# Kernel tuning notes

Measured on AMD Instinct MI355X. Metric: run time of the kernel, lower is better.

The kernel has to match this reference:

```python
import jax, jax.numpy as jnp
import numpy as np
from jax import lax

N_QUBITS = 4
N_QLAYERS = 2
C64 = jnp.complex64
PAIRS = [(i, j) for i in range(N_QUBITS) for j in range(i + 1, N_QUBITS)]  # 6 entangling pairs
CNOT = jnp.array([[1, 0, 0, 0], [0, 1, 0, 0], [0, 0, 0, 1], [0, 0, 1, 0]], dtype=C64)


def _rx(t):
    c = jnp.cos(t / 2).astype(C64)
    s = (-1j * jnp.sin(t / 2)).astype(C64)
    return jnp.stack([jnp.stack([c, s]), jnp.stack([s, c])])


def _ry(t):
    c = jnp.cos(t / 2).astype(C64)
    s = jnp.sin(t / 2).astype(C64)
    return jnp.stack([jnp.stack([c, -s]), jnp.stack([s, c])])


def _rz(t):
    e = jnp.exp(-1j * t.astype(C64) / 2)
    z = jnp.zeros_like(e)
    return jnp.stack([jnp.stack([e, z]), jnp.stack([z, jnp.conj(e)])])


def _apply_1q(state, M, w):
    # state: (B,2,2,2,2); M: (2,2) shared or (B,2,2) per-sample
    s = jnp.moveaxis(state, 1 + w, -1)
    if M.ndim == 2:
        s = jnp.einsum('b...j,ij->b...i', s, M)
    else:
        s = jnp.einsum('b...j,bij->b...i', s, M)
    return jnp.moveaxis(s, -1, 1 + w)


def _apply_2q(state, M4, c, t):
    # M4: (4,4) acting on (wire c, wire t)
    s = jnp.moveaxis(state, (1 + c, 1 + t), (-2, -1))
    sh = s.shape
    s = s.reshape(sh[:-2] + (4,))
    s = jnp.einsum('b...j,ij->b...i', s, M4)
    s = s.reshape(sh)
    return jnp.moveaxis(s, (-2, -1), (1 + c, 1 + t))


def _quantum_batched(angles, q_params):
    # angles: (B, 4) classical outputs; encoding is RY(angles*pi)
    B = angles.shape[0]
    state = jnp.zeros((B, 16), C64).at[:, 0].set(1.0).reshape(B, 2, 2, 2, 2)
    theta = angles * jnp.float32(np.pi)
    c = jnp.cos(theta / 2).astype(C64)  # (B,4)
    s = jnp.sin(theta / 2).astype(C64)
    for w in range(N_QUBITS):
        M = jnp.stack([jnp.stack([c[:, w], -s[:, w]], -1),
                       jnp.stack([s[:, w], c[:, w]], -1)], -2)  # (B,2,2)
        state = _apply_1q(state, M, w)
    per_layer = 3 * N_QUBITS + len(PAIRS)  # 18
    for l in range(N_QLAYERS):
        start = l * per_layer
        rot = q_params[start:start + 3 * N_QUBITS].reshape(N_QUBITS, 3)
        ent = q_params[start + 3 * N_QUBITS:start + per_layer]
        for q in range(N_QUBITS):
            M = _rz(rot[q, 2]) @ _ry(rot[q, 1]) @ _rx(rot[q, 0])
            state = _apply_1q(state, M, q)
        for k, (i, j) in enumerate(PAIRS):
            M4 = jnp.kron(jnp.eye(2, dtype=C64), _rz(ent[k])) @ CNOT  # CNOT then RZ on target
            state = _apply_2q(state, M4, i, j)
    probs = jnp.abs(state) ** 2  # (B,2,2,2,2)
    signs = jnp.array([1.0, -1.0], jnp.float32)
    zs = []
    for w in range(N_QUBITS):
        pw = jnp.moveaxis(probs, 1 + w, -1).reshape(B, -1, 2)
        zs.append((pw.sum(1) * signs).sum(-1))
    return jnp.stack(zs, -1)  # (B,4) PauliZ expvals


def _conv(x, w, b):
    y = lax.conv_general_dilated(x, w, (1, 1), ((1, 1), (1, 1)),
                                 dimension_numbers=('NCHW', 'OIHW', 'NCHW'))
    return y + b[None, :, None, None]


def _pool(x):
    return lax.reduce_window(x, -jnp.inf, lax.max, (1, 1, 2, 2), (1, 1, 2, 2), 'VALID')


def setup_inputs() -> dict:
    key = jax.random.key(0)
    ks = jax.random.split(key, 10)
    B = 4096
    return {
        'x': jax.random.normal(ks[0], (B, 1, 28, 28), jnp.float32),
        'conv1_w': jax.random.normal(ks[1], (16, 1, 3, 3), jnp.float32) * 0.1,
        'conv1_b': jax.random.normal(ks[2], (16,), jnp.float32) * 0.1,
        'conv2_w': jax.random.normal(ks[3], (32, 16, 3, 3), jnp.float32) * 0.05,
        'conv2_b': jax.random.normal(ks[4], (32,), jnp.float32) * 0.1,
        'dense_w': jax.random.normal(ks[5], (4, 1568), jnp.float32) * 0.02,
        'dense_b': jax.random.normal(ks[6], (4,), jnp.float32) * 0.1,
        'q_params': jax.random.normal(ks[7], (36,), jnp.float32) * 0.1,
        'post_w': jax.random.normal(ks[8], (10, 4), jnp.float32) * 0.5,
        'post_b': jax.random.normal(ks[9], (10,), jnp.float32) * 0.1,
    }


def reference(x, conv1_w, conv1_b, conv2_w, conv2_b, dense_w, dense_b, q_params, post_w, post_b):
    h = jax.nn.relu(_conv(x, conv1_w, conv1_b))
    h = _pool(h)
    h = jax.nn.relu(_conv(h, conv2_w, conv2_b))
    h = _pool(h)  # (B,32,7,7)
    h = h.reshape(h.shape[0], 32 * 7 * 7)
    # dropout is identity in eval mode
    angles = h @ dense_w.T + dense_b  # (B,4)
    z = _quantum_batched(angles, q_params)  # (B,4)
    return z @ post_w.T + post_b  # (B,10)
```

## Files before the change

### kernel.cpp

```cpp
#include <hip/hip_runtime.h>

#define PI_F 3.14159265358979323846f

typedef _Float16 half2v __attribute__((ext_vector_type(2)));
typedef _Float16 half4v __attribute__((ext_vector_type(4)));
typedef _Float16 half8v __attribute__((ext_vector_type(8)));
typedef float f32x4 __attribute__((ext_vector_type(4)));

struct C2 { float x, y; };
__device__ __forceinline__ C2 cmul(C2 a, C2 b) {
    return C2{a.x * b.x - a.y * b.y, a.x * b.y + a.y * b.x};
}

__device__ __forceinline__ void gate1(float& re, float& im, int l, int w,
                                      C2 m00, C2 m01, C2 m10, C2 m11) {
    int mask = 1 << (3 - w);
    float pre = __shfl_xor(re, mask, 64);
    float pim = __shfl_xor(im, mask, 64);
    bool b = (l & mask) != 0;
    C2 d = b ? m11 : m00;
    C2 o = b ? m10 : m01;
    float nre = d.x * re - d.y * im + o.x * pre - o.y * pim;
    float nim = d.x * im + d.y * re + o.x * pim + o.y * pre;
    re = nre; im = nim;
}

#define WS_C1B 2560
#define WS_GROT 2688
#define WS_GENT 2752

__global__ __launch_bounds__(256) void qnn_prep(
    const float* __restrict__ w1g, const float* __restrict__ w2g,
    const float* __restrict__ qpg, float* __restrict__ ws)
{
    int t = threadIdx.x;
    for (int e = t; e < 640; e += 256) {
        int kstep = e >> 7, rem = e & 127;
        int ntile = rem >> 6, lane = rem & 63;
        int kq = lane >> 4, n = lane & 15;
        int oc = ntile * 16 + n;
        int pi = kstep * 2 + (kq >> 1);
        half8v h;
        #pragma unroll
        for (int jj = 0; jj < 8; ++jj) {
            int ic = (kq & 1) * 8 + jj;
            float v = (pi < 9) ? w2g[oc * 144 + ic * 9 + pi] : 0.f;
            h[jj] = (_Float16)v;
        }
        *(float4*)(ws + e * 4) = __builtin_bit_cast(float4, h);
    }
    if (t < 64) {
        int ky = t >> 4, n = t & 15;
        half4v h;
        #pragma unroll
        for (int j = 0; j < 4; ++j) {
            float v = (ky < 3 && j < 3) ? w1g[n * 9 + ky * 3 + j] : 0.f;
            h[j] = (_Float16)v;
        }
        *(float2*)(ws + WS_C1B + t * 2) = __builtin_bit_cast(float2, h);
    }
    if (t < 8) {
        int layer = t >> 2, q = t & 3;
        int st = layer * 18;
        float a0 = qpg[st + 3 * q], a1 = qpg[st + 3 * q + 1], a2 = qpg[st + 3 * q + 2];
        float cx = cosf(0.5f * a0), sx = sinf(0.5f * a0);
        float cy = cosf(0.5f * a1), sy = sinf(0.5f * a1);
        float cz = cosf(0.5f * a2), sz = sinf(0.5f * a2);
        C2 T00{cy * cx,  sy * sx}, T01{-sy * cx, -cy * sx};
        C2 T10{sy * cx, -cy * sx}, T11{ cy * cx, -sy * sx};
        C2 E0{cz, -sz}, E1{cz, sz};
        C2 m00 = cmul(E0, T00), m01 = cmul(E0, T01);
        C2 m10 = cmul(E1, T10), m11 = cmul(E1, T11);
        float* gm = ws + WS_GROT + t * 8;
        gm[0] = m00.x; gm[1] = m00.y; gm[2] = m01.x; gm[3] = m01.y;
        gm[4] = m10.x; gm[5] = m10.y; gm[6] = m11.x; gm[7] = m11.y;
    }
    if (t >= 32 && t < 44) {
        int k = t - 32;
        float e = qpg[(k / 6) * 18 + 12 + (k % 6)];
        ws[WS_GENT + k * 2]     = cosf(0.5f * e);
        ws[WS_GENT + k * 2 + 1] = sinf(0.5f * e);
    }
}

__global__ __launch_bounds__(256, 5) void qnn_fused(
    const float* __restrict__ xg,
    const float* __restrict__ b1g, const float* __restrict__ b2g,
    const float* __restrict__ dwg, const float* __restrict__ dbg,
    const float* __restrict__ wsc,
    const float* __restrict__ pwg, const float* __restrict__ pbg,
    float* __restrict__ out)
{
    const int b = blockIdx.x;
    const int t = threadIdx.x;
    const int lane = t & 63;
    const int wv = __builtin_amdgcn_readfirstlane(t >> 6);
    const int kq = lane >> 4;
    const int lm = lane & 15;

    __shared__ __align__(16) unsigned xhl[930];
    __shared__ __align__(16) _Float16 p1f[16 * 20 * 16];
    __shared__ __align__(16) float p2[1568];
    __shared__ float ang[4];
    __shared__ float zsh[4];

    half8v bC2[5][2];
    {
        const float4* wsB = (const float4*)wsc;
        #pragma unroll
        for (int ks = 0; ks < 5; ++ks)
            #pragma unroll
            for (int nt = 0; nt < 2; ++nt)
                bC2[ks][nt] = __builtin_bit_cast(half8v, wsB[(ks * 2 + nt) * 64 + lane]);
    }
    half4v bC1 = __builtin_bit_cast(half4v, *(const float2*)(wsc + WS_C1B + lane * 2));
    float bias1 = b1g[lm];
    float b20 = b2g[lm], b21 = b2g[16 + lm];

    const float* xb = xg + (size_t)b * 784;
    for (int j = t; j < 900; j += 256) {
        int y = j / 30, x = j - y * 30;
        float v = 0.f;
        if (y >= 1 && y <= 28 && x >= 1 && x <= 28)
            v = xb[(y - 1) * 28 + (x - 1)];
        _Float16 h = (_Float16)v;
        _Float16 l = (_Float16)(v - (float)h);
        half2v p; p.x = h; p.y = l;
        xhl[j] = __builtin_bit_cast(unsigned, p);
    }
    if (t < 30) xhl[900 + t] = 0u;
    {
        uint4 z4 = {0u, 0u, 0u, 0u};
        uint4* p4 = (uint4*)p1f;
        #pragma unroll
        for (int j = 0; j < 3; ++j) {
            int i = t + j * 256;
            if (i < 640) p4[i] = z4;
        }
    }
    __syncthreads();

    {
        int kyc = (kq < 3) ? kq : 0;
        for (int tile = wv; tile < 49; tile += 4) {
            int m = tile * 16 + lm;
            int p14 = m >> 2, pos = m & 3;
            int Y = p14 / 14, X = p14 - Y * 14;
            int py = 2 * Y + (pos >> 1), px = 2 * X + (pos & 1);
            int base = (py + kyc) * 30 + px;
            unsigned u0 = xhl[base], u1 = xhl[base + 1], u2 = xhl[base + 2], u3 = xhl[base + 3];
            half2v h0 = __builtin_bit_cast(half2v, u0);
            half2v h1 = __builtin_bit_cast(half2v, u1);
            half2v h2 = __builtin_bit_cast(half2v, u2);
            half2v h3 = __builtin_bit_cast(half2v, u3);
            half4v ah = {h0.x, h1.x, h2.x, h3.x};
            half4v al = {h0.y, h1.y, h2.y, h3.y};
            f32x4 acc = {bias1, bias1, bias1, bias1};
            acc = __builtin_amdgcn_mfma_f32_16x16x16f16(ah, bC1, acc, 0, 0, 0);
            acc = __builtin_amdgcn_mfma_f32_16x16x16f16(al, bC1, acc, 0, 0, 0);
            float v = fmaxf(fmaxf(acc.x, acc.y), fmaxf(acc.z, acc.w));
            v = fmaxf(v, 0.f);
            int q14 = tile * 4 + kq;
            int r = q14 / 14, c = q14 - r * 14;
            p1f[((r + 1) * 20 + (c + 1)) * 16 + lm] = (_Float16)v;
        }
    }
    __syncthreads();

    {
        for (int tile = wv; tile < 13; tile += 4) {
            int m = tile * 16 + lm;
            int quad = m >> 2; if (quad > 48) quad = 48;
            int pos = m & 3;
            int Y = quad / 7, X = quad - Y * 7;
            int py = 2 * Y + (pos >> 1), px = 2 * X + (pos & 1);
            int base0 = py * 20 + px;
            f32x4 acc0 = {b20, b20, b20, b20};
            f32x4 acc1 = {b21, b21, b21, b21};
            int ich = (kq & 1) * 8;
            #pragma unroll
            for (int ks = 0; ks < 5; ++ks) {
                int pi = ks * 2 + (kq >> 1);
                if (pi > 8) pi = 8;
                int ky = (pi >= 6) ? 2 : ((pi >= 3) ? 1 : 0);
                int kx = pi - ky * 3;
                half8v a = *(const half8v*)(&p1f[(base0 + ky * 20 + kx) * 16 + ich]);
                acc0 = __builtin_amdgcn_mfma_f32_16x16x32_f16(a, bC2[ks][0], acc0, 0, 0, 0);
                acc1 = __builtin_amdgcn_mfma_f32_16x16x32_f16(a, bC2[ks][1], acc1, 0, 0, 0);
            }
            int quadO = tile * 4 + kq;
            if (quadO < 49) {
                float v0 = fmaxf(fmaxf(acc0.x, acc0.y), fmaxf(acc0.z, acc0.w));
                float v1 = fmaxf(fmaxf(acc1.x, acc1.y), fmaxf(acc1.z, acc1.w));
                p2[lm * 49 + quadO]        = fmaxf(v0, 0.f);
                p2[(16 + lm) * 49 + quadO] = fmaxf(v1, 0.f);
            }
        }
    }
    __syncthreads();

    {
        int w = t >> 6;
        const float* dw = dwg + w * 1568;
        float partial = 0.f;
        for (int i = lane; i < 1568; i += 64)
            partial = fmaf(p2[i], dw[i], partial);
        #pragma unroll
        for (int m = 32; m >= 1; m >>= 1)
            partial += __shfl_xor(partial, m, 64);
        if (lane == 0) ang[w] = partial + dbg[w];
    }
    __syncthreads();

    if (t < 64) {
        int l = t & 15;
        float re = (l == 0) ? 1.f : 0.f;
        float im = 0.f;
        #pragma unroll
        for (int w = 0; w < 4; ++w) {
            float th = ang[w] * (PI_F * 0.5f);
            float c = cosf(th), s = sinf(th);
            gate1(re, im, l, w, C2{c, 0.f}, C2{-s, 0.f}, C2{s, 0.f}, C2{c, 0.f});
        }
        #pragma unroll
        for (int layer = 0; layer < 2; ++layer) {
            #pragma unroll
            for (int q = 0; q < 4; ++q) {
                const float* gm = wsc + WS_GROT + (layer * 4 + q) * 8;
                gate1(re, im, l, q, C2{gm[0], gm[1]}, C2{gm[2], gm[3]},
                                     C2{gm[4], gm[5]}, C2{gm[6], gm[7]});
            }
            const int pi_[6] = {0, 0, 0, 1, 1, 2};
            const int pj_[6] = {1, 2, 3, 2, 3, 3};
            #pragma unroll
            for (int k = 0; k < 6; ++k) {
                int i = pi_[k], j = pj_[k];
                const float* em = wsc + WS_GENT + (layer * 6 + k) * 2;
                float ce = em[0], se = em[1];
                int maskj = 1 << (3 - j);
                float pre = __shfl_xor(re, maskj, 64);
                float pim = __shfl_xor(im, maskj, 64);
                bool bi = ((l >> (3 - i)) & 1) != 0;
                re = bi ? pre : re;
                im = bi ? pim : im;
                bool bj = (l & maskj) != 0;
                C2 ph{ce, bj ? se : -se};
                C2 r = cmul(C2{re, im}, ph);
                re = r.x; im = r.y;
            }
        }
        float pr = re * re + im * im;
        float z0 = ((l >> 3) & 1) ? -pr : pr;
        float z1 = ((l >> 2) & 1) ? -pr : pr;
        float z2 = ((l >> 1) & 1) ? -pr : pr;
        float z3 = (l & 1)        ? -pr : pr;
        #pragma unroll
        for (int m = 1; m <= 8; m <<= 1) {
            z0 += __shfl_xor(z0, m, 64);
            z1 += __shfl_xor(z1, m, 64);
            z2 += __shfl_xor(z2, m, 64);
            z3 += __shfl_xor(z3, m, 64);
        }
        if (t == 0) { zsh[0] = z0; zsh[1] = z1; zsh[2] = z2; zsh[3] = z3; }
    }
    __syncthreads();

    if (t < 10) {
        float o = pbg[t];
        #pragma unroll
        for (int w = 0; w < 4; ++w)
            o = fmaf(zsh[w], pwg[t * 4 + w], o);
        out[(size_t)b * 10 + t] = o;
    }
}

extern "C" void kernel_launch(void* const* d_in, const int* in_sizes, int n_in,
                              void* d_out, int out_size, void* d_ws, size_t ws_size,
                              hipStream_t stream) {
    const float* x  = (const float*)d_in[0];
    const float* w1 = (const float*)d_in[1];
    const float* b1 = (const float*)d_in[2];
    const float* w2 = (const float*)d_in[3];
    const float* b2 = (const float*)d_in[4];
    const float* dw = (const float*)d_in[5];
    const float* db = (const float*)d_in[6];
    const float* qp = (const float*)d_in[7];
    const float* pw = (const float*)d_in[8];
    const float* pb = (const float*)d_in[9];
    float* out = (float*)d_out;
    float* ws  = (float*)d_ws;
    int B = in_sizes[0] / 784;

    qnn_prep<<<1, 256, 0, stream>>>(w1, w2, qp, ws);
    qnn_fused<<<B, 256, 0, stream>>>(x, b1, b2, dw, db, ws, pw, pb, out);
}
```

Measured before the change: 130.0 us.

## Fuse dense layer into conv2 epilogue with pre-transposed weights, drop p2 buffer

```diff
diff --git a/kernel.cpp b/kernel.cpp
--- a/kernel.cpp
+++ b/kernel.cpp
@@ -26,12 +26,14 @@
 }
 
 #define WS_C1B 2560
-#define WS_GROT 2688
-#define WS_GENT 2752
+#define WS_DWT 2688
+#define WS_GROT 8960
+#define WS_GENT 9024
 
 __global__ __launch_bounds__(256) void qnn_prep(
     const float* __restrict__ w1g, const float* __restrict__ w2g,
-    const float* __restrict__ qpg, float* __restrict__ ws)
+    const float* __restrict__ dwg, const float* __restrict__ qpg,
+    float* __restrict__ ws)
 {
     int t = threadIdx.x;
     for (int e = t; e < 640; e += 256) {
@@ -58,6 +60,10 @@
             h[j] = (_Float16)v;
         }
         *(float2*)(ws + WS_C1B + t * 2) = __builtin_bit_cast(float2, h);
+    }
+    for (int e = t; e < 1568; e += 256) {
+        float4 v = {dwg[e], dwg[1568 + e], dwg[3136 + e], dwg[4704 + e]};
+        *(float4*)(ws + WS_DWT + e * 4) = v;
     }
     if (t < 8) {
         int layer = t >> 2, q = t & 3;
@@ -83,10 +89,10 @@
     }
 }
 
-__global__ __launch_bounds__(256, 5) void qnn_fused(
+__global__ __launch_bounds__(256, 6) void qnn_fused(
     const float* __restrict__ xg,
     const float* __restrict__ b1g, const float* __restrict__ b2g,
-    const float* __restrict__ dwg, const float* __restrict__ dbg,
+    const float* __restrict__ dbg,
     const float* __restrict__ wsc,
     const float* __restrict__ pwg, const float* __restrict__ pbg,
     float* __restrict__ out)
@@ -100,9 +106,7 @@
 
     __shared__ __align__(16) unsigned xhl[930];
     __shared__ __align__(16) _Float16 p1f[16 * 20 * 16];
-    __shared__ __align__(16) float p2[1568];
-    __shared__ float ang[4];
-    __shared__ float zsh[4];
+    __shared__ __align__(16) float angp[16];
 
     half8v bC2[5][2];
     {
@@ -142,11 +146,14 @@
 
     {
         int kyc = (kq < 3) ? kq : 0;
+        int pos = lm & 3;
+        int pyo = pos >> 1, pxo = pos & 1;
+        int p14 = wv * 4 + (lm >> 2);
+        int Y = p14 / 14, X = p14 - Y * 14;
+        int q14 = wv * 4 + kq;
+        int r = q14 / 14, c = q14 - r * 14;
         for (int tile = wv; tile < 49; tile += 4) {
-            int m = tile * 16 + lm;
-            int p14 = m >> 2, pos = m & 3;
-            int Y = p14 / 14, X = p14 - Y * 14;
-            int py = 2 * Y + (pos >> 1), px = 2 * X + (pos & 1);
+            int py = 2 * Y + pyo, px = 2 * X + pxo;
             int base = (py + kyc) * 30 + px;
             unsigned u0 = xhl[base], u1 = xhl[base + 1], u2 = xhl[base + 2], u3 = xhl[base + 3];
             half2v h0 = __builtin_bit_cast(half2v, u0);
@@ -160,14 +167,16 @@
             acc = __builtin_amdgcn_mfma_f32_16x16x16f16(al, bC1, acc, 0, 0, 0);
             float v = fmaxf(fmaxf(acc.x, acc.y), fmaxf(acc.z, acc.w));
             v = fmaxf(v, 0.f);
-            int q14 = tile * 4 + kq;
-            int r = q14 / 14, c = q14 - r * 14;
             p1f[((r + 1) * 20 + (c + 1)) * 16 + lm] = (_Float16)v;
+            X += 2; Y += 1; if (X >= 14) { X -= 14; Y += 1; }
+            c += 2; r += 1; if (c >= 14) { c -= 14; r += 1; }
         }
     }
     __syncthreads();
 
     {
+        float dp0 = 0.f, dp1 = 0.f, dp2 = 0.f, dp3 = 0.f;
+        const float4* dt = (const float4*)(wsc + WS_DWT);
         for (int tile = wv; tile < 13; tile += 4) {
             int m = tile * 16 + lm;
             int quad = m >> 2; if (quad > 48) quad = 48;
@@ -190,35 +199,45 @@
             }
             int quadO = tile * 4 + kq;
             if (quadO < 49) {
-                float v0 = fmaxf(fmaxf(acc0.x, acc0.y), fmaxf(acc0.z, acc0.w));
-                float v1 = fmaxf(fmaxf(acc1.x, acc1.y), fmaxf(acc1.z, acc1.w));
-                p2[lm * 49 + quadO]        = fmaxf(v0, 0.f);
-                p2[(16 + lm) * 49 + quadO] = fmaxf(v1, 0.f);
+                float v0 = fmaxf(fmaxf(fmaxf(acc0.x, acc0.y), fmaxf(acc0.z, acc0.w)), 0.f);
+                float v1 = fmaxf(fmaxf(fmaxf(acc1.x, acc1.y), fmaxf(acc1.z, acc1.w)), 0.f);
+                float4 q0 = dt[lm * 49 + quadO];
+                float4 q1 = dt[(16 + lm) * 49 + quadO];
+                dp0 = fmaf(v0, q0.x, fmaf(v1, q1.x, dp0));
+                dp1 = fmaf(v0, q0.y, fmaf(v1, q1.y, dp1));
+                dp2 = fmaf(v0, q0.z, fmaf(v1, q1.z, dp2));
+                dp3 = fmaf(v0, q0.w, fmaf(v1, q1.w, dp3));
             }
         }
+        #pragma unroll
+        for (int m = 32; m >= 1; m >>= 1) {
+            dp0 += __shfl_xor(dp0, m, 64);
+            dp1 += __shfl_xor(dp1, m, 64);
+            dp2 += __shfl_xor(dp2, m, 64);
+            dp3 += __shfl_xor(dp3, m, 64);
+        }
+        if (lane == 0) {
+            float4 dpv = {dp0, dp1, dp2, dp3};
+            *(float4*)&angp[wv * 4] = dpv;
+        }
     }
     __syncthreads();
 
-    {
-        int w = t >> 6;
-        const float* dw = dwg + w * 1568;
-        float partial = 0.f;
-        for (int i = lane; i < 1568; i += 64)
-            partial = fmaf(p2[i], dw[i], partial);
-        #pragma unroll
-        for (int m = 32; m >= 1; m >>= 1)
-            partial += __shfl_xor(partial, m, 64);
-        if (lane == 0) ang[w] = partial + dbg[w];
-    }
-    __syncthreads();
-
     if (t < 64) {
+        float4 a0v = *(const float4*)&angp[0];
+        float4 a1v = *(const float4*)&angp[4];
+        float4 a2v = *(const float4*)&angp[8];
+        float4 a3v = *(const float4*)&angp[12];
+        float aw[4] = {a0v.x + a1v.x + a2v.x + a3v.x + dbg[0],
+                       a0v.y + a1v.y + a2v.y + a3v.y + dbg[1],
+                       a0v.z + a1v.z + a2v.z + a3v.z + dbg[2],
+                       a0v.w + a1v.w + a2v.w + a3v.w + dbg[3]};
         int l = t & 15;
         float re = (l == 0) ? 1.f : 0.f;
         float im = 0.f;
         #pragma unroll
         for (int w = 0; w < 4; ++w) {
-            float th = ang[w] * (PI_F * 0.5f);
+            float th = aw[w] * (PI_F * 0.5f);
             float c = cosf(th), s = sinf(th);
             gate1(re, im, l, w, C2{c, 0.f}, C2{-s, 0.f}, C2{s, 0.f}, C2{c, 0.f});
         }
@@ -261,16 +280,13 @@
             z2 += __shfl_xor(z2, m, 64);
             z3 += __shfl_xor(z3, m, 64);
         }
-        if (t == 0) { zsh[0] = z0; zsh[1] = z1; zsh[2] = z2; zsh[3] = z3; }
-    }
-    __syncthreads();
-
-    if (t < 10) {
-        float o = pbg[t];
-        #pragma unroll
-        for (int w = 0; w < 4; ++w)
-            o = fmaf(zsh[w], pwg[t * 4 + w], o);
-        out[(size_t)b * 10 + t] = o;
+        if (t < 10) {
+            float4 pw4 = *(const float4*)(pwg + t * 4);
+            float o = pbg[t];
+            o = fmaf(z0, pw4.x, o); o = fmaf(z1, pw4.y, o);
+            o = fmaf(z2, pw4.z, o); o = fmaf(z3, pw4.w, o);
+            out[(size_t)b * 10 + t] = o;
+        }
     }
 }
 
@@ -291,6 +307,6 @@
     float* ws  = (float*)d_ws;
     int B = in_sizes[0] / 784;
 
-    qnn_prep<<<1, 256, 0, stream>>>(w1, w2, qp, ws);
-    qnn_fused<<<B, 256, 0, stream>>>(x, b1, b2, dw, db, ws, pw, pb, out);
-}
+    qnn_prep<<<1, 256, 0, stream>>>(w1, w2, dw, qp, ws);
+    qnn_fused<<<B, 256, 0, stream>>>(x, b1, b2, db, ws, pw, pb, out);
+}
```

Measured after the change: 117.7 us. 1.1x faster.
